# Kernel optimization log

Measured on AMD Instinct MI355X. Metric: run time of the kernel, lower is better.

Reference implementation:

```python
import jax, jax.numpy as jnp
import numpy as np

N, E, P = 50000, 400000, 3
DIN, H, O, HID = 128, 8, 32, 128
NEG_SLOPE = 0.2


def setup_inputs() -> dict:
    key = jax.random.key(0)
    ks = jax.random.split(key, 9)
    feat = jax.random.normal(ks[0], (N, DIN), dtype=jnp.float32)
    edges = jax.random.randint(ks[1], (P, 2, E), 0, N, dtype=jnp.int64)
    Ws = jax.random.normal(ks[2], (P, DIN, H * O), dtype=jnp.float32) * (1.0 / np.sqrt(DIN))
    attn_l = jax.random.normal(ks[3], (P, H, O), dtype=jnp.float32) * 0.1
    attn_r = jax.random.normal(ks[4], (P, H, O), dtype=jnp.float32) * 0.1
    bias = jnp.zeros((P, H * O), dtype=jnp.float32)
    sem_W1 = jax.random.normal(ks[5], (H * O, HID), dtype=jnp.float32) * (1.0 / np.sqrt(H * O))
    sem_b1 = jnp.zeros((HID,), dtype=jnp.float32)
    sem_w2 = jax.random.normal(ks[6], (HID,), dtype=jnp.float32) * (1.0 / np.sqrt(HID))
    return {"feat": feat, "edges": edges, "Ws": Ws, "attn_l": attn_l,
            "attn_r": attn_r, "bias": bias, "sem_W1": sem_W1,
            "sem_b1": sem_b1, "sem_w2": sem_w2}


def _gat_conv(feat, src, dst, W, al, ar, b):
    n = feat.shape[0]
    h = (feat @ W).reshape(n, H, O)                       # [N,H,O]
    el = jnp.sum(h * al, axis=-1)                         # [N,H]
    er = jnp.sum(h * ar, axis=-1)                         # [N,H]
    e = jax.nn.leaky_relu(el[src] + er[dst], NEG_SLOPE)   # [E,H]
    # segment softmax over incoming edges of each dst node
    m = jax.ops.segment_max(e, dst, num_segments=n)
    e = jnp.exp(e - jax.lax.stop_gradient(m)[dst])
    s = jax.ops.segment_sum(e, dst, num_segments=n)
    alpha = e / s[dst]                                    # [E,H]
    out = jax.ops.segment_sum(alpha[:, :, None] * h[src], dst, num_segments=n)
    return jax.nn.elu(out.reshape(n, H * O) + b)          # [N,H*O]


def reference(feat, edges, Ws, attn_l, attn_r, bias, sem_W1, sem_b1, sem_w2):
    zs = []
    for p in range(P):
        zs.append(_gat_conv(feat, edges[p, 0], edges[p, 1],
                            Ws[p], attn_l[p], attn_r[p], bias[p]))
    z = jnp.stack(zs, axis=1)                             # [N,P,H*O]
    # semantic attention: project -> mean over nodes -> softmax over paths
    w = jnp.tanh(z @ sem_W1 + sem_b1) @ sem_w2            # [N,P]
    beta = jax.nn.softmax(jnp.mean(w, axis=0))            # [P]
    return jnp.sum(beta[None, :, None] * z, axis=1)       # [N,H*O]
```

## Files before the change

### kernel.cpp

```cpp
#include <hip/hip_runtime.h>


#define N_NODES 50000
#define N_EDGES 400000
#define N_PATHS 3
#define DIN     128
#define NH      8
#define NO      32
#define NC      256
#define HID     128
#define CAP     32

typedef __bf16    bf16x8 __attribute__((ext_vector_type(8)));
typedef _Float16  half8  __attribute__((ext_vector_type(8)));
typedef float     f32x4  __attribute__((ext_vector_type(4)));

__device__ __forceinline__ float bf2f(unsigned short u) {
    return __uint_as_float(((unsigned int)u) << 16);
}
__device__ __forceinline__ unsigned short f2bf(float f) {
    unsigned int u = __float_as_uint(f);
    unsigned int r = u + 0x7FFFu + ((u >> 16) & 1u);
    return (unsigned short)(r >> 16);
}
__device__ __forceinline__ unsigned short hbits(_Float16 h) {
    return *(unsigned short*)&h;
}
__device__ __forceinline__ float fast_tanh(float x) {
    x = fminf(fmaxf(x, -15.f), 15.f);
    float e = __expf(2.f * x);
    return (e - 1.f) * __builtin_amdgcn_rcpf(e + 1.f);
}

__global__ void prep_wt(const float* __restrict__ Ws,
                        unsigned short* __restrict__ wt_hi,
                        unsigned short* __restrict__ wt_lo) {
    int idx = blockIdx.x * 256 + threadIdx.x;
    if (idx >= N_PATHS * DIN * NC) return;
    int p   = idx / (DIN * NC);
    int rem = idx - p * (DIN * NC);
    int k = rem >> 8;
    int c = rem & 255;
    float x = Ws[idx];
    _Float16 h = (_Float16)x;
    _Float16 l = (_Float16)(x - (float)h);
    int o = p * (DIN * NC) + c * DIN + k;
    wt_hi[o] = hbits(h);
    wt_lo[o] = hbits(l);
}

__global__ __launch_bounds__(256) void gemm_node(
    const float* __restrict__ feat, const unsigned short* __restrict__ wt_hi,
    const unsigned short* __restrict__ wt_lo,
    const float* __restrict__ al, const float* __restrict__ ar,
    unsigned short* __restrict__ hbuf, float* __restrict__ el,
    float* __restrict__ er, int p) {
    int n0 = blockIdx.x * 64;
    int cy = blockIdx.y;
    int t = threadIdx.x;
    int w    = t >> 6;
    int lane = t & 63;
    int cid  = lane & 15;
    int kgrp = lane >> 4;

    __shared__ unsigned short sBh[128 * 40];
    __shared__ unsigned short sBl[128 * 40];

    f32x4 acc[8];
#pragma unroll
    for (int ct = 0; ct < 8; ++ct) acc[ct] = (f32x4){0.f, 0.f, 0.f, 0.f};

    const unsigned short* bhsrc = wt_hi + ((size_t)p * NC + cy * 128) * DIN;
    const unsigned short* blsrc = wt_lo + ((size_t)p * NC + cy * 128) * DIN;

    int myrow = n0 + w * 16 + cid;
    if (myrow >= N_NODES) myrow = N_NODES - 1;
    const float* fr = feat + (size_t)myrow * DIN;

    for (int k0 = 0; k0 < DIN; k0 += 32) {
        float4 v0 = *(const float4*)(fr + k0 + kgrp * 8);
        float4 v1 = *(const float4*)(fr + k0 + kgrp * 8 + 4);
#pragma unroll
        for (int i = 0; i < 2; ++i) {
            int q = i * 256 + t;
            int col = q >> 2;
            int kq = (q & 3) * 8;
            *(uint4*)(sBh + col * 40 + kq) =
                *(const uint4*)(bhsrc + (size_t)col * DIN + k0 + kq);
            *(uint4*)(sBl + col * 40 + kq) =
                *(const uint4*)(blsrc + (size_t)col * DIN + k0 + kq);
        }
        __syncthreads();

        half8 ahi, alo;
        {
            _Float16 h0 = (_Float16)v0.x, h1 = (_Float16)v0.y,
                     h2 = (_Float16)v0.z, h3 = (_Float16)v0.w,
                     h4 = (_Float16)v1.x, h5 = (_Float16)v1.y,
                     h6 = (_Float16)v1.z, h7 = (_Float16)v1.w;
            ahi[0] = h0; ahi[1] = h1; ahi[2] = h2; ahi[3] = h3;
            ahi[4] = h4; ahi[5] = h5; ahi[6] = h6; ahi[7] = h7;
            alo[0] = (_Float16)(v0.x - (float)h0);
            alo[1] = (_Float16)(v0.y - (float)h1);
            alo[2] = (_Float16)(v0.z - (float)h2);
            alo[3] = (_Float16)(v0.w - (float)h3);
            alo[4] = (_Float16)(v1.x - (float)h4);
            alo[5] = (_Float16)(v1.y - (float)h5);
            alo[6] = (_Float16)(v1.z - (float)h6);
            alo[7] = (_Float16)(v1.w - (float)h7);
        }
        int koff = kgrp * 8;
#pragma unroll
        for (int ct = 0; ct < 8; ++ct) {
            half8 bhi = *(const half8*)(sBh + (ct * 16 + cid) * 40 + koff);
            half8 blo = *(const half8*)(sBl + (ct * 16 + cid) * 40 + koff);
            acc[ct] = __builtin_amdgcn_mfma_f32_16x16x32_f16(ahi, bhi, acc[ct], 0, 0, 0);
            acc[ct] = __builtin_amdgcn_mfma_f32_16x16x32_f16(ahi, blo, acc[ct], 0, 0, 0);
            acc[ct] = __builtin_amdgcn_mfma_f32_16x16x32_f16(alo, bhi, acc[ct], 0, 0, 0);
        }
        __syncthreads();
    }

    float psl[4][4], psr[4][4];
#pragma unroll
    for (int hh = 0; hh < 4; ++hh)
#pragma unroll
        for (int r = 0; r < 4; ++r) { psl[hh][r] = 0.f; psr[hh][r] = 0.f; }

#pragma unroll
    for (int ct = 0; ct < 8; ++ct) {
        int o = (ct & 1) * 16 + cid;
        int head = cy * 4 + (ct >> 1);
        float av = al[(p * NH + head) * NO + o];
        float rv = ar[(p * NH + head) * NO + o];
#pragma unroll
        for (int r = 0; r < 4; ++r) {
            float v = acc[ct][r];
            psl[ct >> 1][r] += v * av;
            psr[ct >> 1][r] += v * rv;
        }
    }
#pragma unroll
    for (int m = 1; m < 16; m <<= 1) {
#pragma unroll
        for (int hh = 0; hh < 4; ++hh)
#pragma unroll
            for (int r = 0; r < 4; ++r) {
                psl[hh][r] += __shfl_xor(psl[hh][r], m, 64);
                psr[hh][r] += __shfl_xor(psr[hh][r], m, 64);
            }
    }

#pragma unroll
    for (int r = 0; r < 4; ++r) {
        int node = n0 + w * 16 + kgrp * 4 + r;
        if (node < N_NODES) {
            unsigned short* hb = hbuf + (size_t)node * NC + cy * 128;
#pragma unroll
            for (int ct = 0; ct < 8; ++ct)
                hb[ct * 16 + cid] = f2bf(acc[ct][r]);
        }
    }
    if (cid == 0) {
#pragma unroll
        for (int r = 0; r < 4; ++r) {
            int node = n0 + w * 16 + kgrp * 4 + r;
            if (node < N_NODES) {
#pragma unroll
                for (int hh = 0; hh < 4; ++hh) {
                    el[(size_t)node * NH + cy * 4 + hh] = psl[hh][r];
                    er[(size_t)node * NH + cy * 4 + hh] = psr[hh][r];
                }
            }
        }
    }
}

__global__ void fill_bucket(const int* __restrict__ edges_p, int* __restrict__ cnt,
                            int* __restrict__ csrb) {
    int e = blockIdx.x * 256 + threadIdx.x;
    if (e >= N_EDGES) return;
    int src = edges_p[e];
    int dst = edges_p[N_EDGES + e];
    int pos = atomicAdd(&cnt[dst], 1);
    if (pos < CAP) csrb[(size_t)dst * CAP + pos] = src;
}

__global__ __launch_bounds__(256) void phase_ab(
    const int* __restrict__ csrb, const int* __restrict__ cnt,
    const float* __restrict__ el, const float* __restrict__ er,
    const unsigned short* __restrict__ hbuf, const float* __restrict__ bias,
    unsigned short* __restrict__ zbuf, int p) {
    int t = threadIdx.x;
    int ld = t >> 5;
    int sl = t & 31;
    int dst = blockIdx.x * 8 + ld;
    if (dst >= N_NODES) return;
    int c0 = sl * 8;
    int hd = sl >> 2;
    int d   = cnt[dst];
    d = (d < CAP) ? d : CAP;
    const int* cp = csrb + (size_t)dst * CAP;
    float erv = er[(size_t)dst * NH + hd];

    float s = 0.f;
    float acc[8];
#pragma unroll
    for (int i = 0; i < 8; ++i) acc[i] = 0.f;

    int j = 0;
    for (; j + 2 <= d; j += 2) {
        int s0 = cp[j], s1 = cp[j + 1];
        float x0 = el[(size_t)s0 * NH + hd] + erv;
        float x1 = el[(size_t)s1 * NH + hd] + erv;
        uint4 h0 = *(const uint4*)(hbuf + (size_t)s0 * NC + c0);
        uint4 h1 = *(const uint4*)(hbuf + (size_t)s1 * NC + c0);
        x0 = (x0 >= 0.f) ? x0 : 0.2f * x0;
        x1 = (x1 >= 0.f) ? x1 : 0.2f * x1;
        float e0 = __expf(x0);
        float e1 = __expf(x1);
        s += e0 + e1;
        acc[0] += e0 * bf2f((unsigned short)(h0.x & 0xffffu))
                + e1 * bf2f((unsigned short)(h1.x & 0xffffu));
        acc[1] += e0 * bf2f((unsigned short)(h0.x >> 16))
                + e1 * bf2f((unsigned short)(h1.x >> 16));
        acc[2] += e0 * bf2f((unsigned short)(h0.y & 0xffffu))
                + e1 * bf2f((unsigned short)(h1.y & 0xffffu));
        acc[3] += e0 * bf2f((unsigned short)(h0.y >> 16))
                + e1 * bf2f((unsigned short)(h1.y >> 16));
        acc[4] += e0 * bf2f((unsigned short)(h0.z & 0xffffu))
                + e1 * bf2f((unsigned short)(h1.z & 0xffffu));
        acc[5] += e0 * bf2f((unsigned short)(h0.z >> 16))
                + e1 * bf2f((unsigned short)(h1.z >> 16));
        acc[6] += e0 * bf2f((unsigned short)(h0.w & 0xffffu))
                + e1 * bf2f((unsigned short)(h1.w & 0xffffu));
        acc[7] += e0 * bf2f((unsigned short)(h0.w >> 16))
                + e1 * bf2f((unsigned short)(h1.w >> 16));
    }
    if (j < d) {
        int s0 = cp[j];
        float x0 = el[(size_t)s0 * NH + hd] + erv;
        uint4 h0 = *(const uint4*)(hbuf + (size_t)s0 * NC + c0);
        x0 = (x0 >= 0.f) ? x0 : 0.2f * x0;
        float e0 = __expf(x0);
        s += e0;
        acc[0] += e0 * bf2f((unsigned short)(h0.x & 0xffffu));
        acc[1] += e0 * bf2f((unsigned short)(h0.x >> 16));
        acc[2] += e0 * bf2f((unsigned short)(h0.y & 0xffffu));
        acc[3] += e0 * bf2f((unsigned short)(h0.y >> 16));
        acc[4] += e0 * bf2f((unsigned short)(h0.z & 0xffffu));
        acc[5] += e0 * bf2f((unsigned short)(h0.z >> 16));
        acc[6] += e0 * bf2f((unsigned short)(h0.w & 0xffffu));
        acc[7] += e0 * bf2f((unsigned short)(h0.w >> 16));
    }
    float rsv = (d > 0) ? 1.0f / s : 0.f;

    const float* bp = bias + p * NC + c0;
    unsigned short* zp = zbuf + ((size_t)p * N_NODES + dst) * NC + c0;
    float o[8];
#pragma unroll
    for (int i = 0; i < 8; ++i) {
        float zv = acc[i] * rsv + bp[i];
        o[i] = (zv > 0.f) ? zv : (__expf(zv) - 1.f);
    }
    uint4 pk;
    pk.x = (unsigned int)f2bf(o[0]) | ((unsigned int)f2bf(o[1]) << 16);
    pk.y = (unsigned int)f2bf(o[2]) | ((unsigned int)f2bf(o[3]) << 16);
    pk.z = (unsigned int)f2bf(o[4]) | ((unsigned int)f2bf(o[5]) << 16);
    pk.w = (unsigned int)f2bf(o[6]) | ((unsigned int)f2bf(o[7]) << 16);
    *(uint4*)zp = pk;
}

__global__ void prep_w1t(const float* __restrict__ W1, unsigned short* __restrict__ w1t) {
    int idx = blockIdx.x * 256 + threadIdx.x;
    int k = idx >> 7;
    int j = idx & 127;
    w1t[j * NC + k] = f2bf(W1[idx]);
}

__global__ __launch_bounds__(256) void semantic(
    const unsigned short* __restrict__ zbuf, const unsigned short* __restrict__ w1t,
    const float* __restrict__ b1, const float* __restrict__ w2,
    float* __restrict__ wpart) {
    int p  = blockIdx.y;
    int n0 = blockIdx.x * 64;
    int t  = threadIdx.x;
    int w    = t >> 6;
    int lane = t & 63;
    int cid  = lane & 15;
    int kgrp = lane >> 4;

    __shared__ unsigned short w1s[128 * 72];
    __shared__ float red[16];

    f32x4 acc[8];
#pragma unroll
    for (int ct = 0; ct < 8; ++ct) acc[ct] = (f32x4){0.f, 0.f, 0.f, 0.f};

    int myrow = n0 + w * 16 + cid;
    if (myrow >= N_NODES) myrow = N_NODES - 1;
    const unsigned short* zr = zbuf + ((size_t)p * N_NODES + myrow) * NC;

    for (int k0 = 0; k0 < NC; k0 += 64) {
        bf16x8 a0 = *(const bf16x8*)(zr + k0 + kgrp * 8);
        bf16x8 a1 = *(const bf16x8*)(zr + k0 + 32 + kgrp * 8);
#pragma unroll
        for (int i = 0; i < 4; ++i) {
            int q = i * 256 + t;
            int j = q >> 3;
            int kq = (q & 7) * 8;
            *(uint4*)(w1s + j * 72 + kq) =
                *(const uint4*)(w1t + (size_t)j * NC + k0 + kq);
        }
        __syncthreads();

        int koff = kgrp * 8;
#pragma unroll
        for (int ct = 0; ct < 8; ++ct) {
            bf16x8 b = *(const bf16x8*)(w1s + (ct * 16 + cid) * 72 + koff);
            acc[ct] = __builtin_amdgcn_mfma_f32_16x16x32_bf16(a0, b, acc[ct], 0, 0, 0);
        }
#pragma unroll
        for (int ct = 0; ct < 8; ++ct) {
            bf16x8 b = *(const bf16x8*)(w1s + (ct * 16 + cid) * 72 + 32 + koff);
            acc[ct] = __builtin_amdgcn_mfma_f32_16x16x32_bf16(a1, b, acc[ct], 0, 0, 0);
        }
        __syncthreads();
    }

    float psum[4] = {0.f, 0.f, 0.f, 0.f};
#pragma unroll
    for (int ct = 0; ct < 8; ++ct) {
        int col = ct * 16 + cid;
        float bb = b1[col], wv = w2[col];
#pragma unroll
        for (int r = 0; r < 4; ++r)
            psum[r] += fast_tanh(acc[ct][r] + bb) * wv;
    }
#pragma unroll
    for (int m = 1; m < 16; m <<= 1) {
#pragma unroll
        for (int r = 0; r < 4; ++r)
            psum[r] += __shfl_xor(psum[r], m, 64);
    }
    if (cid == 0) {
        int rowb = n0 + w * 16 + kgrp * 4;
        float s = 0.f;
#pragma unroll
        for (int r = 0; r < 4; ++r)
            if (rowb + r < N_NODES) s += psum[r];
        red[w * 4 + kgrp] = s;
    }
    __syncthreads();
    if (t == 0) {
        float s = 0.f;
#pragma unroll
        for (int i = 0; i < 16; ++i) s += red[i];
        atomicAdd(&wpart[p * 256 + (blockIdx.x & 255)], s);
    }
}

__global__ void compute_beta(const float* __restrict__ wpart, float* __restrict__ beta) {
    __shared__ float s[256];
    int t = threadIdx.x;
    float m[N_PATHS];
    for (int p = 0; p < N_PATHS; ++p) {
        s[t] = wpart[p * 256 + t];
        __syncthreads();
        for (int off = 128; off > 0; off >>= 1) {
            if (t < off) s[t] += s[t + off];
            __syncthreads();
        }
        m[p] = s[0] / (float)N_NODES;
        __syncthreads();
    }
    if (t == 0) {
        float mx = fmaxf(m[0], fmaxf(m[1], m[2]));
        float e0 = expf(m[0] - mx), e1 = expf(m[1] - mx), e2 = expf(m[2] - mx);
        float inv = 1.f / (e0 + e1 + e2);
        beta[0] = e0 * inv; beta[1] = e1 * inv; beta[2] = e2 * inv;
    }
}

__global__ __launch_bounds__(256) void final_mix(
    const unsigned short* __restrict__ zbuf, const float* __restrict__ beta,
    float* __restrict__ out) {
    int idx8 = blockIdx.x * 256 + threadIdx.x;
    size_t base = (size_t)idx8 * 8;
    if (base >= (size_t)N_NODES * NC) return;
    float b0 = beta[0], b1 = beta[1], b2 = beta[2];
    size_t stride = (size_t)N_NODES * NC;
    uint4 z0 = *(const uint4*)(zbuf + base);
    uint4 z1 = *(const uint4*)(zbuf + base + stride);
    uint4 z2 = *(const uint4*)(zbuf + base + 2 * stride);
    float o[8];
    const unsigned int* u0 = (const unsigned int*)&z0;
    const unsigned int* u1 = (const unsigned int*)&z1;
    const unsigned int* u2 = (const unsigned int*)&z2;
#pragma unroll
    for (int i = 0; i < 4; ++i) {
        o[2*i]   = b0 * bf2f((unsigned short)(u0[i] & 0xffffu))
                 + b1 * bf2f((unsigned short)(u1[i] & 0xffffu))
                 + b2 * bf2f((unsigned short)(u2[i] & 0xffffu));
        o[2*i+1] = b0 * bf2f((unsigned short)(u0[i] >> 16))
                 + b1 * bf2f((unsigned short)(u1[i] >> 16))
                 + b2 * bf2f((unsigned short)(u2[i] >> 16));
    }
    *(float4*)(out + base)     = make_float4(o[0], o[1], o[2], o[3]);
    *(float4*)(out + base + 4) = make_float4(o[4], o[5], o[6], o[7]);
}

extern "C" void kernel_launch(void* const* d_in, const int* in_sizes, int n_in,
                              void* d_out, int out_size, void* d_ws, size_t ws_size,
                              hipStream_t stream) {
    const float* feat  = (const float*)d_in[0];
    const int*   edges = (const int*)d_in[1];
    const float* Ws    = (const float*)d_in[2];
    const float* al    = (const float*)d_in[3];
    const float* ar    = (const float*)d_in[4];
    const float* bias  = (const float*)d_in[5];
    const float* W1    = (const float*)d_in[6];
    const float* b1    = (const float*)d_in[7];
    const float* w2    = (const float*)d_in[8];
    float* out = (float*)d_out;

    size_t off = 0;
    auto alloc = [&](size_t bytes) { size_t o = off; off += (bytes + 255) & ~(size_t)255; return o; };
    size_t zbuf_o  = alloc((size_t)N_PATHS * N_NODES * NC * 2);
    size_t hbuf_o  = alloc((size_t)N_NODES * NC * 2);
    size_t el_o    = alloc((size_t)N_NODES * NH * 4);
    size_t er_o    = alloc((size_t)N_NODES * NH * 4);
    size_t csrb_o  = alloc((size_t)N_NODES * CAP * 4);
    size_t beta_o  = alloc(256);
    size_t cnt3_o  = alloc((size_t)N_PATHS * N_NODES * 4);
    size_t zend_o  = off;
    size_t wpart_o = alloc((size_t)N_PATHS * 256 * 4);
    size_t w1t_o   = alloc((size_t)HID * NC * 2);
    size_t wth_o   = alloc((size_t)N_PATHS * NC * DIN * 2);
    size_t wtl_o   = alloc((size_t)N_PATHS * NC * DIN * 2);
    size_t total = off;
    if (ws_size < total) return;

    char* ws = (char*)d_ws;
    unsigned short* zbuf  = (unsigned short*)(ws + zbuf_o);
    unsigned short* hbuf  = (unsigned short*)(ws + hbuf_o);
    float* el    = (float*)(ws + el_o);
    float* er    = (float*)(ws + er_o);
    int*   csrb  = (int*)(ws + csrb_o);
    float* beta  = (float*)(ws + beta_o);
    int*   cnt3  = (int*)(ws + cnt3_o);
    float* wpart = (float*)(ws + wpart_o);
    unsigned short* w1t   = (unsigned short*)(ws + w1t_o);
    unsigned short* wt_hi = (unsigned short*)(ws + wth_o);
    unsigned short* wt_lo = (unsigned short*)(ws + wtl_o);

    hipMemsetAsync(ws + wpart_o, 0, (size_t)N_PATHS * 256 * 4, stream);
    hipMemsetAsync(ws + cnt3_o, 0, zend_o - cnt3_o, stream);
    prep_w1t<<<128, 256, 0, stream>>>(W1, w1t);
    prep_wt<<<(N_PATHS * DIN * NC + 255) / 256, 256, 0, stream>>>(Ws, wt_hi, wt_lo);

    for (int p = 0; p < N_PATHS; ++p) {
        const int* edges_p = edges + (size_t)p * 2 * N_EDGES;
        fill_bucket<<<(N_EDGES + 255) / 256, 256, 0, stream>>>(
            edges_p, cnt3 + (size_t)p * N_NODES, csrb);
        gemm_node<<<dim3((N_NODES + 63) / 64, 2), 256, 0, stream>>>(
            feat, wt_hi, wt_lo, al, ar, hbuf, el, er, p);
        phase_ab<<<(N_NODES + 7) / 8, 256, 0, stream>>>(
            csrb, cnt3 + (size_t)p * N_NODES, el, er, hbuf, bias, zbuf, p);
    }
    semantic<<<dim3((N_NODES + 63) / 64, N_PATHS), 256, 0, stream>>>(
        zbuf, w1t, b1, w2, wpart);
    compute_beta<<<1, 256, 0, stream>>>(wpart, beta);
    final_mix<<<(N_NODES * NC / 8 + 255) / 256, 256, 0, stream>>>(zbuf, beta, out);
}
```

Baseline: 426.3 us.

## Batch all metapaths into single launches with per-path buffers and unroll gather by four

Replaces the per-path loop of fill_bucket, gemm_node and phase_ab launches with single launches that index the path by a grid dimension. hbuf, el, er and csrb become per-path buffers, so the three paths can run at the same time. The two prep kernels merge into one, the two memsets merge into one, and the phase_ab gather loop now unrolls by four with a vectorized int4 index load. The aim is fewer launches, less tail idle time between small kernels and more memory-level parallelism in the gather, at the cost of a larger workspace and a bigger cache footprint.

```diff
diff --git a/kernel.cpp b/kernel.cpp
--- a/kernel.cpp
+++ b/kernel.cpp
@@ -31,37 +31,60 @@
     float e = __expf(2.f * x);
     return (e - 1.f) * __builtin_amdgcn_rcpf(e + 1.f);
 }
-
-__global__ void prep_wt(const float* __restrict__ Ws,
-                        unsigned short* __restrict__ wt_hi,
-                        unsigned short* __restrict__ wt_lo) {
+__device__ __forceinline__ void acc8(float* acc, float e, uint4 h) {
+    acc[0] += e * bf2f((unsigned short)(h.x & 0xffffu));
+    acc[1] += e * bf2f((unsigned short)(h.x >> 16));
+    acc[2] += e * bf2f((unsigned short)(h.y & 0xffffu));
+    acc[3] += e * bf2f((unsigned short)(h.y >> 16));
+    acc[4] += e * bf2f((unsigned short)(h.z & 0xffffu));
+    acc[5] += e * bf2f((unsigned short)(h.z >> 16));
+    acc[6] += e * bf2f((unsigned short)(h.w & 0xffffu));
+    acc[7] += e * bf2f((unsigned short)(h.w >> 16));
+}
+
+__global__ void prep_all(const float* __restrict__ Ws, const float* __restrict__ W1,
+                         unsigned short* __restrict__ wt_hi,
+                         unsigned short* __restrict__ wt_lo,
+                         unsigned short* __restrict__ w1t) {
     int idx = blockIdx.x * 256 + threadIdx.x;
-    if (idx >= N_PATHS * DIN * NC) return;
-    int p   = idx / (DIN * NC);
-    int rem = idx - p * (DIN * NC);
-    int k = rem >> 8;
-    int c = rem & 255;
-    float x = Ws[idx];
-    _Float16 h = (_Float16)x;
-    _Float16 l = (_Float16)(x - (float)h);
-    int o = p * (DIN * NC) + c * DIN + k;
-    wt_hi[o] = hbits(h);
-    wt_lo[o] = hbits(l);
-}
-
-__global__ __launch_bounds__(256) void gemm_node(
+    const int NWT = N_PATHS * DIN * NC;
+    if (idx < NWT) {
+        int p   = idx / (DIN * NC);
+        int rem = idx - p * (DIN * NC);
+        int k = rem >> 8;
+        int c = rem & 255;
+        float x = Ws[idx];
+        _Float16 h = (_Float16)x;
+        _Float16 l = (_Float16)(x - (float)h);
+        int o = p * (DIN * NC) + c * DIN + k;
+        wt_hi[o] = hbits(h);
+        wt_lo[o] = hbits(l);
+    } else if (idx < NWT + NC * HID) {
+        int i2 = idx - NWT;
+        int k = i2 >> 7;
+        int j = i2 & 127;
+        w1t[j * NC + k] = f2bf(W1[i2]);
+    }
+}
+
+__global__ __launch_bounds__(256) void gemm_node_all(
     const float* __restrict__ feat, const unsigned short* __restrict__ wt_hi,
     const unsigned short* __restrict__ wt_lo,
     const float* __restrict__ al, const float* __restrict__ ar,
-    unsigned short* __restrict__ hbuf, float* __restrict__ el,
-    float* __restrict__ er, int p) {
+    unsigned short* __restrict__ hbuf3, float* __restrict__ el3,
+    float* __restrict__ er3) {
     int n0 = blockIdx.x * 64;
     int cy = blockIdx.y;
+    int p  = blockIdx.z;
     int t = threadIdx.x;
     int w    = t >> 6;
     int lane = t & 63;
     int cid  = lane & 15;
     int kgrp = lane >> 4;
+
+    unsigned short* hbuf = hbuf3 + (size_t)p * N_NODES * NC;
+    float* el = el3 + (size_t)p * N_NODES * NH;
+    float* er = er3 + (size_t)p * N_NODES * NH;
 
     __shared__ unsigned short sBh[128 * 40];
     __shared__ unsigned short sBl[128 * 40];
@@ -176,31 +199,40 @@
     }
 }
 
-__global__ void fill_bucket(const int* __restrict__ edges_p, int* __restrict__ cnt,
-                            int* __restrict__ csrb) {
+__global__ void fill_bucket_all(const int* __restrict__ edges, int* __restrict__ cnt3,
+                                int* __restrict__ csrb3) {
     int e = blockIdx.x * 256 + threadIdx.x;
+    int p = blockIdx.y;
     if (e >= N_EDGES) return;
-    int src = edges_p[e];
-    int dst = edges_p[N_EDGES + e];
-    int pos = atomicAdd(&cnt[dst], 1);
-    if (pos < CAP) csrb[(size_t)dst * CAP + pos] = src;
-}
-
-__global__ __launch_bounds__(256) void phase_ab(
-    const int* __restrict__ csrb, const int* __restrict__ cnt,
-    const float* __restrict__ el, const float* __restrict__ er,
-    const unsigned short* __restrict__ hbuf, const float* __restrict__ bias,
-    unsigned short* __restrict__ zbuf, int p) {
+    const int* ep = edges + (size_t)p * 2 * N_EDGES;
+    int src = ep[e];
+    int dst = ep[N_EDGES + e];
+    int pos = atomicAdd(&cnt3[p * N_NODES + dst], 1);
+    if (pos < CAP)
+        csrb3[((size_t)p * N_NODES + dst) * CAP + pos] = src;
+}
+
+__global__ __launch_bounds__(256) void phase_ab_all(
+    const int* __restrict__ csrb3, const int* __restrict__ cnt3,
+    const float* __restrict__ el3, const float* __restrict__ er3,
+    const unsigned short* __restrict__ hbuf3, const float* __restrict__ bias,
+    unsigned short* __restrict__ zbuf) {
     int t = threadIdx.x;
+    int p = blockIdx.y;
     int ld = t >> 5;
     int sl = t & 31;
     int dst = blockIdx.x * 8 + ld;
     if (dst >= N_NODES) return;
     int c0 = sl * 8;
     int hd = sl >> 2;
-    int d   = cnt[dst];
+
+    const float* el = el3 + (size_t)p * N_NODES * NH;
+    const float* er = er3 + (size_t)p * N_NODES * NH;
+    const unsigned short* hbuf = hbuf3 + (size_t)p * N_NODES * NC;
+
+    int d = cnt3[p * N_NODES + dst];
     d = (d < CAP) ? d : CAP;
-    const int* cp = csrb + (size_t)dst * CAP;
+    const int* cp = csrb3 + ((size_t)p * N_NODES + dst) * CAP;
     float erv = er[(size_t)dst * NH + hd];
 
     float s = 0.f;
@@ -209,49 +241,36 @@
     for (int i = 0; i < 8; ++i) acc[i] = 0.f;
 
     int j = 0;
-    for (; j + 2 <= d; j += 2) {
-        int s0 = cp[j], s1 = cp[j + 1];
-        float x0 = el[(size_t)s0 * NH + hd] + erv;
-        float x1 = el[(size_t)s1 * NH + hd] + erv;
-        uint4 h0 = *(const uint4*)(hbuf + (size_t)s0 * NC + c0);
-        uint4 h1 = *(const uint4*)(hbuf + (size_t)s1 * NC + c0);
-        x0 = (x0 >= 0.f) ? x0 : 0.2f * x0;
-        x1 = (x1 >= 0.f) ? x1 : 0.2f * x1;
-        float e0 = __expf(x0);
-        float e1 = __expf(x1);
-        s += e0 + e1;
-        acc[0] += e0 * bf2f((unsigned short)(h0.x & 0xffffu))
-                + e1 * bf2f((unsigned short)(h1.x & 0xffffu));
-        acc[1] += e0 * bf2f((unsigned short)(h0.x >> 16))
-                + e1 * bf2f((unsigned short)(h1.x >> 16));
-        acc[2] += e0 * bf2f((unsigned short)(h0.y & 0xffffu))
-                + e1 * bf2f((unsigned short)(h1.y & 0xffffu));
-        acc[3] += e0 * bf2f((unsigned short)(h0.y >> 16))
-                + e1 * bf2f((unsigned short)(h1.y >> 16));
-        acc[4] += e0 * bf2f((unsigned short)(h0.z & 0xffffu))
-                + e1 * bf2f((unsigned short)(h1.z & 0xffffu));
-        acc[5] += e0 * bf2f((unsigned short)(h0.z >> 16))
-                + e1 * bf2f((unsigned short)(h1.z >> 16));
-        acc[6] += e0 * bf2f((unsigned short)(h0.w & 0xffffu))
-                + e1 * bf2f((unsigned short)(h1.w & 0xffffu));
-        acc[7] += e0 * bf2f((unsigned short)(h0.w >> 16))
-                + e1 * bf2f((unsigned short)(h1.w >> 16));
-    }
-    if (j < d) {
+    for (; j + 4 <= d; j += 4) {
+        int4 ii = *(const int4*)(cp + j);
+        float xa = el[(size_t)ii.x * NH + hd] + erv;
+        float xb = el[(size_t)ii.y * NH + hd] + erv;
+        float xc = el[(size_t)ii.z * NH + hd] + erv;
+        float xd = el[(size_t)ii.w * NH + hd] + erv;
+        uint4 hA = *(const uint4*)(hbuf + (size_t)ii.x * NC + c0);
+        uint4 hB = *(const uint4*)(hbuf + (size_t)ii.y * NC + c0);
+        uint4 hC = *(const uint4*)(hbuf + (size_t)ii.z * NC + c0);
+        uint4 hD = *(const uint4*)(hbuf + (size_t)ii.w * NC + c0);
+        xa = (xa >= 0.f) ? xa : 0.2f * xa;
+        xb = (xb >= 0.f) ? xb : 0.2f * xb;
+        xc = (xc >= 0.f) ? xc : 0.2f * xc;
+        xd = (xd >= 0.f) ? xd : 0.2f * xd;
+        float ea = __expf(xa), eb = __expf(xb);
+        float ec = __expf(xc), ed = __expf(xd);
+        s += (ea + eb) + (ec + ed);
+        acc8(acc, ea, hA);
+        acc8(acc, eb, hB);
+        acc8(acc, ec, hC);
+        acc8(acc, ed, hD);
+    }
+    for (; j < d; ++j) {
         int s0 = cp[j];
         float x0 = el[(size_t)s0 * NH + hd] + erv;
         uint4 h0 = *(const uint4*)(hbuf + (size_t)s0 * NC + c0);
         x0 = (x0 >= 0.f) ? x0 : 0.2f * x0;
         float e0 = __expf(x0);
         s += e0;
-        acc[0] += e0 * bf2f((unsigned short)(h0.x & 0xffffu));
-        acc[1] += e0 * bf2f((unsigned short)(h0.x >> 16));
-        acc[2] += e0 * bf2f((unsigned short)(h0.y & 0xffffu));
-        acc[3] += e0 * bf2f((unsigned short)(h0.y >> 16));
-        acc[4] += e0 * bf2f((unsigned short)(h0.z & 0xffffu));
-        acc[5] += e0 * bf2f((unsigned short)(h0.z >> 16));
-        acc[6] += e0 * bf2f((unsigned short)(h0.w & 0xffffu));
-        acc[7] += e0 * bf2f((unsigned short)(h0.w >> 16));
+        acc8(acc, e0, h0);
     }
     float rsv = (d > 0) ? 1.0f / s : 0.f;
 
@@ -269,13 +288,6 @@
     pk.z = (unsigned int)f2bf(o[4]) | ((unsigned int)f2bf(o[5]) << 16);
     pk.w = (unsigned int)f2bf(o[6]) | ((unsigned int)f2bf(o[7]) << 16);
     *(uint4*)zp = pk;
-}
-
-__global__ void prep_w1t(const float* __restrict__ W1, unsigned short* __restrict__ w1t) {
-    int idx = blockIdx.x * 256 + threadIdx.x;
-    int k = idx >> 7;
-    int j = idx & 127;
-    w1t[j * NC + k] = f2bf(W1[idx]);
 }
 
 __global__ __launch_bounds__(256) void semantic(
@@ -427,14 +439,14 @@
     size_t off = 0;
     auto alloc = [&](size_t bytes) { size_t o = off; off += (bytes + 255) & ~(size_t)255; return o; };
     size_t zbuf_o  = alloc((size_t)N_PATHS * N_NODES * NC * 2);
-    size_t hbuf_o  = alloc((size_t)N_NODES * NC * 2);
-    size_t el_o    = alloc((size_t)N_NODES * NH * 4);
-    size_t er_o    = alloc((size_t)N_NODES * NH * 4);
-    size_t csrb_o  = alloc((size_t)N_NODES * CAP * 4);
+    size_t hbuf3_o = alloc((size_t)N_PATHS * N_NODES * NC * 2);
+    size_t el3_o   = alloc((size_t)N_PATHS * N_NODES * NH * 4);
+    size_t er3_o   = alloc((size_t)N_PATHS * N_NODES * NH * 4);
+    size_t csrb3_o = alloc((size_t)N_PATHS * N_NODES * CAP * 4);
     size_t beta_o  = alloc(256);
     size_t cnt3_o  = alloc((size_t)N_PATHS * N_NODES * 4);
+    size_t wpart_o = alloc((size_t)N_PATHS * 256 * 4);
     size_t zend_o  = off;
-    size_t wpart_o = alloc((size_t)N_PATHS * 256 * 4);
     size_t w1t_o   = alloc((size_t)HID * NC * 2);
     size_t wth_o   = alloc((size_t)N_PATHS * NC * DIN * 2);
     size_t wtl_o   = alloc((size_t)N_PATHS * NC * DIN * 2);
@@ -443,10 +455,10 @@
 
     char* ws = (char*)d_ws;
     unsigned short* zbuf  = (unsigned short*)(ws + zbuf_o);
-    unsigned short* hbuf  = (unsigned short*)(ws + hbuf_o);
-    float* el    = (float*)(ws + el_o);
-    float* er    = (float*)(ws + er_o);
-    int*   csrb  = (int*)(ws + csrb_o);
+    unsigned short* hbuf3 = (unsigned short*)(ws + hbuf3_o);
+    float* el3   = (float*)(ws + el3_o);
+    float* er3   = (float*)(ws + er3_o);
+    int*   csrb3 = (int*)(ws + csrb3_o);
     float* beta  = (float*)(ws + beta_o);
     int*   cnt3  = (int*)(ws + cnt3_o);
     float* wpart = (float*)(ws + wpart_o);
@@ -454,20 +466,17 @@
     unsigned short* wt_hi = (unsigned short*)(ws + wth_o);
     unsigned short* wt_lo = (unsigned short*)(ws + wtl_o);
 
-    hipMemsetAsync(ws + wpart_o, 0, (size_t)N_PATHS * 256 * 4, stream);
     hipMemsetAsync(ws + cnt3_o, 0, zend_o - cnt3_o, stream);
-    prep_w1t<<<128, 256, 0, stream>>>(W1, w1t);
-    prep_wt<<<(N_PATHS * DIN * NC + 255) / 256, 256, 0, stream>>>(Ws, wt_hi, wt_lo);
-
-    for (int p = 0; p < N_PATHS; ++p) {
-        const int* edges_p = edges + (size_t)p * 2 * N_EDGES;
-        fill_bucket<<<(N_EDGES + 255) / 256, 256, 0, stream>>>(
-            edges_p, cnt3 + (size_t)p * N_NODES, csrb);
-        gemm_node<<<dim3((N_NODES + 63) / 64, 2), 256, 0, stream>>>(
-            feat, wt_hi, wt_lo, al, ar, hbuf, el, er, p);
-        phase_ab<<<(N_NODES + 7) / 8, 256, 0, stream>>>(
-            csrb, cnt3 + (size_t)p * N_NODES, el, er, hbuf, bias, zbuf, p);
-    }
+
+    const int NPREP = N_PATHS * DIN * NC + NC * HID;
+    prep_all<<<(NPREP + 255) / 256, 256, 0, stream>>>(Ws, W1, wt_hi, wt_lo, w1t);
+
+    fill_bucket_all<<<dim3((N_EDGES + 255) / 256, N_PATHS), 256, 0, stream>>>(
+        edges, cnt3, csrb3);
+    gemm_node_all<<<dim3((N_NODES + 63) / 64, 2, N_PATHS), 256, 0, stream>>>(
+        feat, wt_hi, wt_lo, al, ar, hbuf3, el3, er3);
+    phase_ab_all<<<dim3((N_NODES + 7) / 8, N_PATHS), 256, 0, stream>>>(
+        csrb3, cnt3, el3, er3, hbuf3, bias, zbuf);
     semantic<<<dim3((N_NODES + 63) / 64, N_PATHS), 256, 0, stream>>>(
         zbuf, w1t, b1, w2, wpart);
     compute_beta<<<1, 256, 0, stream>>>(wpart, beta);
```

Result: faster. 406.9 us, median of 2 (-4.5%).
